# Performance work log

Measured on AMD Instinct MI355X. Metric: run time of the kernel, lower is better.

Reference implementation:

```python
import jax, jax.numpy as jnp
import numpy as np

N = 320      # points per coordinate axis
RANK = 64    # CP rank = features[-1]
H = 128      # hidden width
DIMS = 3     # input_dim


def setup_inputs() -> dict:
    key = jax.random.key(0)
    ks = jax.random.split(key, 6)
    s0 = (6.0 / (1 + H)) ** 0.5   # xavier-uniform-ish scale for 1->H
    s1 = (6.0 / (H + H)) ** 0.5
    s2 = (6.0 / (H + RANK)) ** 0.5
    return {
        "xs": jax.random.normal(ks[0], (DIMS, N, 1), dtype=jnp.float32),
        "W0": jax.random.uniform(ks[1], (DIMS, 1, H), jnp.float32, -s0, s0),
        "b0": jnp.zeros((DIMS, H), jnp.float32),
        "W1": jax.random.uniform(ks[2], (DIMS, H, H), jnp.float32, -s1, s1),
        "b1": jnp.zeros((DIMS, H), jnp.float32),
        "W2": jax.random.uniform(ks[3], (DIMS, H, H), jnp.float32, -s1, s1),
        "b2": jnp.zeros((DIMS, H), jnp.float32),
        "W3": jax.random.uniform(ks[4], (DIMS, H, RANK), jnp.float32, -s2, s2),
        "b3": jnp.zeros((DIMS, RANK), jnp.float32),
    }


def reference(xs, W0, b0, W1, b1, W2, b2, W3, b3):
    # Per-coordinate MLP (identical to independent Dense stacks in the flax loop),
    # vmapped over the DIMS leading axis of stacked params.
    def mlp(x, w0, bb0, w1, bb1, w2, bb2, w3, bb3):
        h = jnp.tanh(x @ w0 + bb0)          # (N, H)
        h = jnp.tanh(h @ w1 + bb1)          # (N, H)
        h = jnp.tanh(h @ w2 + bb2)          # (N, H)
        return h @ w3 + bb3                 # (N, R)

    outs = jax.vmap(mlp)(xs, W0, b0, W1, b1, W2, b2, W3, b3)  # (DIMS, N, R)
    f = jnp.transpose(outs, (0, 2, 1))                         # (DIMS, R, N)
    # CP reconstruction: 'ra,rb,rc->abc' over shared rank r
    return jnp.einsum('ra,rb,rc->abc', f[0], f[1], f[2])
```

## Files before the change

### kernel.cpp

```cpp
#include <hip/hip_runtime.h>
#include <math.h>

#define DIMS 3
#define NPTS 320
#define HID  128
#define RANK 64
#define CH   160
#define LROW 256

typedef __attribute__((ext_vector_type(8)))  short bf16x8;
typedef __attribute__((ext_vector_type(16))) float f32x16;

static __device__ __forceinline__ unsigned short f2bf_rn(float x) {
    union { float f; unsigned int u; } v; v.f = x;
    unsigned int r = v.u + 0x7fffu + ((v.u >> 16) & 1u);
    return (unsigned short)(r >> 16);
}
static __device__ __forceinline__ float bf2f(unsigned short h) {
    union { unsigned int u; float f; } v; v.u = ((unsigned int)h) << 16;
    return v.f;
}

__global__ __launch_bounds__(HID)
void mlp_kernel(const float* __restrict__ xs,
                const float* __restrict__ W0, const float* __restrict__ b0,
                const float* __restrict__ W1, const float* __restrict__ b1,
                const float* __restrict__ W2, const float* __restrict__ b2,
                const float* __restrict__ W3, const float* __restrict__ b3,
                float* __restrict__ f01t,
                unsigned short* __restrict__ f2hi,
                unsigned short* __restrict__ f2lo) {
    int blk = blockIdx.x;
    int d = blk / NPTS, n = blk % NPTS;
    int j = threadIdx.x;

    __shared__ float ha[HID];
    __shared__ float hb[HID];

    float x = xs[d * NPTS + n];

    ha[j] = tanhf(fmaf(x, W0[d * HID + j], b0[d * HID + j]));
    __syncthreads();

    {
        float acc = b1[d * HID + j];
        const float* w = W1 + d * HID * HID + j;
        #pragma unroll 16
        for (int k = 0; k < HID; ++k) acc = fmaf(ha[k], w[k * HID], acc);
        hb[j] = tanhf(acc);
    }
    __syncthreads();

    {
        float acc = b2[d * HID + j];
        const float* w = W2 + d * HID * HID + j;
        #pragma unroll 16
        for (int k = 0; k < HID; ++k) acc = fmaf(hb[k], w[k * HID], acc);
        ha[j] = tanhf(acc);
    }
    __syncthreads();

    if (j < RANK) {
        float acc = b3[d * RANK + j];
        const float* w = W3 + d * HID * RANK + j;
        #pragma unroll 16
        for (int k = 0; k < HID; ++k) acc = fmaf(ha[k], w[k * RANK], acc);

        if (d == 0) {
            f01t[n * RANK + j] = acc;
        } else if (d == 1) {
            f01t[(NPTS + n) * RANK + j] = acc;
        } else {
            unsigned short hi = f2bf_rn(acc);
            f2hi[n * RANK + j] = hi;
            f2lo[n * RANK + j] = f2bf_rn(acc - bf2f(hi));
        }
    }
}

__global__ __launch_bounds__(128, 2)
void cp_mfma_kernel(const float* __restrict__ f01t,
                    const unsigned short* __restrict__ f2hi,
                    const unsigned short* __restrict__ f2lo,
                    float* __restrict__ out) {
    const int tx = threadIdx.x;
    const int w  = tx >> 6;
    const int l  = tx & 63;
    const int lc = l & 31;
    const int hw = l >> 5;

    const int chalf = blockIdx.x & 1;
    const int c0 = chalf * CH;

    __shared__ char sB[CH * LROW];

    #pragma unroll
    for (int i = 0; i < 10; ++i) {
        int idx = tx + i * 128;
        int row = idx >> 3;
        int g   = (idx & 7) << 4;
        int sw  = (row & 15) << 4;
        *(float4*)(&sB[row * LROW + (g ^ sw)]) =
            ((const float4*)f2hi)[c0 * 8 + idx];
        *(float4*)(&sB[row * LROW + ((128 + g) ^ sw)]) =
            ((const float4*)f2lo)[c0 * 8 + idx];
    }
    __syncthreads();

    for (int t = blockIdx.x >> 1; t < NPTS * 5; t += 512) {
        const int a    = t / 5;
        const int b0w  = (t - a * 5) * 64 + w * 32;
        const float* f0p = f01t + (size_t)a * RANK + hw * 8;
        const float* f1p = f01t + (size_t)(NPTS + b0w + lc) * RANK + hw * 8;

        bf16x8 ahi[4], alo[4];
        #pragma unroll
        for (int ks = 0; ks < 4; ++ks) {
            const int k0 = ks * 16;
            float4 f0a = *(const float4*)(f0p + k0);
            float4 f0b = *(const float4*)(f0p + k0 + 4);
            float4 f1a = *(const float4*)(f1p + k0);
            float4 f1b = *(const float4*)(f1p + k0 + 4);

            float g[8];
            g[0] = f1a.x * f0a.x; g[1] = f1a.y * f0a.y;
            g[2] = f1a.z * f0a.z; g[3] = f1a.w * f0a.w;
            g[4] = f1b.x * f0b.x; g[5] = f1b.y * f0b.y;
            g[6] = f1b.z * f0b.z; g[7] = f1b.w * f0b.w;

            #pragma unroll
            for (int j = 0; j < 8; ++j) {
                unsigned short hi = f2bf_rn(g[j]);
                ahi[ks][j] = (short)hi;
                alo[ks][j] = (short)f2bf_rn(g[j] - bf2f(hi));
            }
        }

        #pragma unroll
        for (int ct = 0; ct < 5; ++ct) {
            const int lr = ct * 32 + lc;
            const int sw = (lr & 15) << 4;
            const char* rowp = &sB[lr * LROW];

            f32x16 acc;
            #pragma unroll
            for (int j = 0; j < 16; ++j) acc[j] = 0.0f;

            #pragma unroll
            for (int ks = 0; ks < 4; ++ks) {
                const int base = ks * 32 + (hw << 4);
                bf16x8 b_hi = *(const bf16x8*)(rowp + (base ^ sw));
                bf16x8 b_lo = *(const bf16x8*)(rowp + ((128 + base) ^ sw));
                acc = __builtin_amdgcn_mfma_f32_32x32x16_bf16(ahi[ks], b_hi, acc, 0, 0, 0);
                acc = __builtin_amdgcn_mfma_f32_32x32x16_bf16(ahi[ks], b_lo, acc, 0, 0, 0);
                acc = __builtin_amdgcn_mfma_f32_32x32x16_bf16(alo[ks], b_hi, acc, 0, 0, 0);
            }

            float* obase = out + ((size_t)a * NPTS + b0w) * NPTS + c0 + ct * 32 + lc;
            #pragma unroll
            for (int q = 0; q < 16; ++q) {
                int row = (q & 3) + 8 * (q >> 2) + 4 * hw;
                obase[(size_t)row * NPTS] = acc[q];
            }
        }
    }
}

extern "C" void kernel_launch(void* const* d_in, const int* in_sizes, int n_in,
                              void* d_out, int out_size, void* d_ws, size_t ws_size,
                              hipStream_t stream) {
    const float* xs = (const float*)d_in[0];
    const float* W0 = (const float*)d_in[1];
    const float* b0 = (const float*)d_in[2];
    const float* W1 = (const float*)d_in[3];
    const float* b1 = (const float*)d_in[4];
    const float* W2 = (const float*)d_in[5];
    const float* b2 = (const float*)d_in[6];
    const float* W3 = (const float*)d_in[7];
    const float* b3 = (const float*)d_in[8];

    float* f01t = (float*)d_ws;
    unsigned short* f2hi = (unsigned short*)((char*)d_ws + 2 * NPTS * RANK * 4);
    unsigned short* f2lo = f2hi + NPTS * RANK;
    float* out = (float*)d_out;

    mlp_kernel<<<dim3(DIMS * NPTS), dim3(HID), 0, stream>>>(
        xs, W0, b0, W1, b1, W2, b2, W3, b3, f01t, f2hi, f2lo);

    cp_mfma_kernel<<<dim3(1024), dim3(128), 0, stream>>>(f01t, f2hi, f2lo, out);
}
```

Measured before the change: 40.63 us.

## Widen CP blocks to four waves and split tiles contiguously per block

The CP reconstruction kernel now runs 256 threads per block. Each pair of waves covers two adjacent 'a' rows over a 64-wide b tile, so every shared-memory load of the f2 slice serves twice as much work. Blocks take contiguous ranges of tiles instead of a strided loop, which evens the per-block load and keeps output writes local. Two accumulators alternate across the column tiles so one tile's MFMAs can overlap the previous tile's stores, at the cost of more registers per thread.

```diff
diff --git a/kernel.cpp b/kernel.cpp
--- a/kernel.cpp
+++ b/kernel.cpp
@@ -78,25 +78,26 @@
     }
 }
 
-__global__ __launch_bounds__(128, 2)
+__global__ __launch_bounds__(256)
 void cp_mfma_kernel(const float* __restrict__ f01t,
                     const unsigned short* __restrict__ f2hi,
                     const unsigned short* __restrict__ f2lo,
                     float* __restrict__ out) {
     const int tx = threadIdx.x;
     const int w  = tx >> 6;
+    const int aw = w >> 1;
+    const int bw = (w & 1) * 32;
     const int l  = tx & 63;
     const int lc = l & 31;
     const int hw = l >> 5;
 
-    const int chalf = blockIdx.x & 1;
-    const int c0 = chalf * CH;
+    const int c0 = (blockIdx.x & 1) * CH;
 
     __shared__ char sB[CH * LROW];
 
     #pragma unroll
-    for (int i = 0; i < 10; ++i) {
-        int idx = tx + i * 128;
+    for (int i = 0; i < 5; ++i) {
+        int idx = tx + i * 256;
         int row = idx >> 3;
         int g   = (idx & 7) << 4;
         int sw  = (row & 15) << 4;
@@ -107,11 +108,18 @@
     }
     __syncthreads();
 
-    for (int t = blockIdx.x >> 1; t < NPTS * 5; t += 512) {
-        const int a    = t / 5;
-        const int b0w  = (t - a * 5) * 64 + w * 32;
+    const int slot   = blockIdx.x >> 1;
+    const int tstart = (slot * 25) >> 4;
+    const int tend   = ((slot + 1) * 25) >> 4;
+
+    for (int t = tstart; t < tend; ++t) {
+        const int apair = t / 5;
+        const int btile = t - apair * 5;
+        const int a  = apair * 2 + aw;
+        const int bb = btile * 64 + bw;
+
         const float* f0p = f01t + (size_t)a * RANK + hw * 8;
-        const float* f1p = f01t + (size_t)(NPTS + b0w + lc) * RANK + hw * 8;
+        const float* f1p = f01t + (size_t)(NPTS + bb + lc) * RANK + hw * 8;
 
         bf16x8 ahi[4], alo[4];
         #pragma unroll
@@ -136,33 +144,38 @@
             }
         }
 
-        #pragma unroll
-        for (int ct = 0; ct < 5; ++ct) {
-            const int lr = ct * 32 + lc;
-            const int sw = (lr & 15) << 4;
-            const char* rowp = &sB[lr * LROW];
-
-            f32x16 acc;
-            #pragma unroll
-            for (int j = 0; j < 16; ++j) acc[j] = 0.0f;
-
-            #pragma unroll
-            for (int ks = 0; ks < 4; ++ks) {
-                const int base = ks * 32 + (hw << 4);
-                bf16x8 b_hi = *(const bf16x8*)(rowp + (base ^ sw));
-                bf16x8 b_lo = *(const bf16x8*)(rowp + ((128 + base) ^ sw));
-                acc = __builtin_amdgcn_mfma_f32_32x32x16_bf16(ahi[ks], b_hi, acc, 0, 0, 0);
-                acc = __builtin_amdgcn_mfma_f32_32x32x16_bf16(ahi[ks], b_lo, acc, 0, 0, 0);
-                acc = __builtin_amdgcn_mfma_f32_32x32x16_bf16(alo[ks], b_hi, acc, 0, 0, 0);
-            }
-
-            float* obase = out + ((size_t)a * NPTS + b0w) * NPTS + c0 + ct * 32 + lc;
-            #pragma unroll
-            for (int q = 0; q < 16; ++q) {
-                int row = (q & 3) + 8 * (q >> 2) + 4 * hw;
-                obase[(size_t)row * NPTS] = acc[q];
-            }
+        float* obase = out + ((size_t)a * NPTS + bb) * NPTS + c0 + lc;
+
+#define CP_STEP(CT, ACC)                                                       \
+        {                                                                      \
+            const int lr = (CT) * 32 + lc;                                     \
+            const int sw2 = (lr & 15) << 4;                                    \
+            const char* rowp = &sB[lr * LROW];                                 \
+            _Pragma("unroll")                                                  \
+            for (int j = 0; j < 16; ++j) ACC[j] = 0.0f;                        \
+            _Pragma("unroll")                                                  \
+            for (int ks = 0; ks < 4; ++ks) {                                   \
+                const int base = ks * 32 + (hw << 4);                          \
+                bf16x8 b_hi = *(const bf16x8*)(rowp + (base ^ sw2));           \
+                bf16x8 b_lo = *(const bf16x8*)(rowp + ((128 + base) ^ sw2));   \
+                ACC = __builtin_amdgcn_mfma_f32_32x32x16_bf16(ahi[ks], b_hi, ACC, 0, 0, 0); \
+                ACC = __builtin_amdgcn_mfma_f32_32x32x16_bf16(ahi[ks], b_lo, ACC, 0, 0, 0); \
+                ACC = __builtin_amdgcn_mfma_f32_32x32x16_bf16(alo[ks], b_hi, ACC, 0, 0, 0); \
+            }                                                                  \
+            _Pragma("unroll")                                                  \
+            for (int q = 0; q < 16; ++q) {                                     \
+                int row = (q & 3) + 8 * (q >> 2) + 4 * hw;                     \
+                obase[(size_t)row * NPTS + (CT) * 32] = ACC[q];                \
+            }                                                                  \
         }
+
+        f32x16 accA, accB;
+        CP_STEP(0, accA)
+        CP_STEP(1, accB)
+        CP_STEP(2, accA)
+        CP_STEP(3, accB)
+        CP_STEP(4, accA)
+#undef CP_STEP
     }
 }
 
@@ -187,5 +200,5 @@
     mlp_kernel<<<dim3(DIMS * NPTS), dim3(HID), 0, stream>>>(
         xs, W0, b0, W1, b1, W2, b2, W3, b3, f01t, f2hi, f2lo);
 
-    cp_mfma_kernel<<<dim3(1024), dim3(128), 0, stream>>>(f01t, f2hi, f2lo, out);
-}
+    cp_mfma_kernel<<<dim3(1024), dim3(256), 0, stream>>>(f01t, f2hi, f2lo, out);
+}
```

Result: slower. 43.81 us (+7.8%).

## Batch MLP points per block and merge CP column halves into one block

Applied to the files above, without the earlier changes.

The MLP kernel now processes four points per block, so each weight load is reused across four accumulators and the block count drops by a factor of four. The CP kernel now uses 256-thread blocks that stage the full factor-2 matrix (80KB LDS) and split the column halves across warps. It also keeps five accumulators live so that all tile stores are issued together after the MFMAs. The costs are higher register pressure, large LDS use that limits occupancy, and fewer MLP blocks for the GPU to spread across its units.

```diff
diff --git a/kernel.cpp b/kernel.cpp
--- a/kernel.cpp
+++ b/kernel.cpp
@@ -5,8 +5,8 @@
 #define NPTS 320
 #define HID  128
 #define RANK 64
-#define CH   160
 #define LROW 256
+#define PB   4
 
 typedef __attribute__((ext_vector_type(8)))  short bf16x8;
 typedef __attribute__((ext_vector_type(16))) float f32x16;
@@ -30,88 +30,117 @@
                 float* __restrict__ f01t,
                 unsigned short* __restrict__ f2hi,
                 unsigned short* __restrict__ f2lo) {
-    int blk = blockIdx.x;
-    int d = blk / NPTS, n = blk % NPTS;
-    int j = threadIdx.x;
-
-    __shared__ float ha[HID];
-    __shared__ float hb[HID];
-
-    float x = xs[d * NPTS + n];
-
-    ha[j] = tanhf(fmaf(x, W0[d * HID + j], b0[d * HID + j]));
-    __syncthreads();
+    const int blk = blockIdx.x;
+    const int d  = blk / (NPTS / PB);
+    const int n0 = (blk - d * (NPTS / PB)) * PB;
+    const int j  = threadIdx.x;
+
+    __shared__ float ha[PB][HID];
+    __shared__ float hb[PB][HID];
+
+    float x[PB];
+    #pragma unroll
+    for (int p = 0; p < PB; ++p) x[p] = xs[d * NPTS + n0 + p];
 
     {
-        float acc = b1[d * HID + j];
+        float w = W0[d * HID + j], bb = b0[d * HID + j];
+        #pragma unroll
+        for (int p = 0; p < PB; ++p) ha[p][j] = tanhf(fmaf(x[p], w, bb));
+    }
+    __syncthreads();
+
+    {
+        float acc[PB];
+        #pragma unroll
+        for (int p = 0; p < PB; ++p) acc[p] = b1[d * HID + j];
         const float* w = W1 + d * HID * HID + j;
-        #pragma unroll 16
-        for (int k = 0; k < HID; ++k) acc = fmaf(ha[k], w[k * HID], acc);
-        hb[j] = tanhf(acc);
+        #pragma unroll 8
+        for (int k = 0; k < HID; ++k) {
+            float wv = w[k * HID];
+            #pragma unroll
+            for (int p = 0; p < PB; ++p) acc[p] = fmaf(ha[p][k], wv, acc[p]);
+        }
+        #pragma unroll
+        for (int p = 0; p < PB; ++p) hb[p][j] = tanhf(acc[p]);
     }
     __syncthreads();
 
     {
-        float acc = b2[d * HID + j];
+        float acc[PB];
+        #pragma unroll
+        for (int p = 0; p < PB; ++p) acc[p] = b2[d * HID + j];
         const float* w = W2 + d * HID * HID + j;
-        #pragma unroll 16
-        for (int k = 0; k < HID; ++k) acc = fmaf(hb[k], w[k * HID], acc);
-        ha[j] = tanhf(acc);
+        #pragma unroll 8
+        for (int k = 0; k < HID; ++k) {
+            float wv = w[k * HID];
+            #pragma unroll
+            for (int p = 0; p < PB; ++p) acc[p] = fmaf(hb[p][k], wv, acc[p]);
+        }
+        __syncthreads();
+        #pragma unroll
+        for (int p = 0; p < PB; ++p) ha[p][j] = tanhf(acc[p]);
     }
     __syncthreads();
 
     if (j < RANK) {
-        float acc = b3[d * RANK + j];
+        float acc[PB];
+        #pragma unroll
+        for (int p = 0; p < PB; ++p) acc[p] = b3[d * RANK + j];
         const float* w = W3 + d * HID * RANK + j;
-        #pragma unroll 16
-        for (int k = 0; k < HID; ++k) acc = fmaf(ha[k], w[k * RANK], acc);
-
-        if (d == 0) {
-            f01t[n * RANK + j] = acc;
-        } else if (d == 1) {
-            f01t[(NPTS + n) * RANK + j] = acc;
-        } else {
-            unsigned short hi = f2bf_rn(acc);
-            f2hi[n * RANK + j] = hi;
-            f2lo[n * RANK + j] = f2bf_rn(acc - bf2f(hi));
-        }
-    }
-}
-
-__global__ __launch_bounds__(128, 2)
+        #pragma unroll 8
+        for (int k = 0; k < HID; ++k) {
+            float wv = w[k * RANK];
+            #pragma unroll
+            for (int p = 0; p < PB; ++p) acc[p] = fmaf(ha[p][k], wv, acc[p]);
+        }
+        #pragma unroll
+        for (int p = 0; p < PB; ++p) {
+            int n = n0 + p;
+            if (d == 0) {
+                f01t[n * RANK + j] = acc[p];
+            } else if (d == 1) {
+                f01t[(NPTS + n) * RANK + j] = acc[p];
+            } else {
+                unsigned short hi = f2bf_rn(acc[p]);
+                f2hi[n * RANK + j] = hi;
+                f2lo[n * RANK + j] = f2bf_rn(acc[p] - bf2f(hi));
+            }
+        }
+    }
+}
+
+__global__ __launch_bounds__(256, 2)
 void cp_mfma_kernel(const float* __restrict__ f01t,
                     const unsigned short* __restrict__ f2hi,
                     const unsigned short* __restrict__ f2lo,
                     float* __restrict__ out) {
     const int tx = threadIdx.x;
     const int w  = tx >> 6;
+    const int bsub  = (w & 1) * 32;
+    const int chalf = (w >> 1) * 160;
     const int l  = tx & 63;
     const int lc = l & 31;
     const int hw = l >> 5;
 
-    const int chalf = blockIdx.x & 1;
-    const int c0 = chalf * CH;
-
-    __shared__ char sB[CH * LROW];
+    __shared__ char sB[NPTS * LROW];
 
     #pragma unroll
     for (int i = 0; i < 10; ++i) {
-        int idx = tx + i * 128;
+        int idx = tx + i * 256;
         int row = idx >> 3;
         int g   = (idx & 7) << 4;
         int sw  = (row & 15) << 4;
-        *(float4*)(&sB[row * LROW + (g ^ sw)]) =
-            ((const float4*)f2hi)[c0 * 8 + idx];
-        *(float4*)(&sB[row * LROW + ((128 + g) ^ sw)]) =
-            ((const float4*)f2lo)[c0 * 8 + idx];
-    }
-    __syncthreads();
-
-    for (int t = blockIdx.x >> 1; t < NPTS * 5; t += 512) {
-        const int a    = t / 5;
-        const int b0w  = (t - a * 5) * 64 + w * 32;
+        *(float4*)(&sB[row * LROW + (g ^ sw)])         = ((const float4*)f2hi)[idx];
+        *(float4*)(&sB[row * LROW + ((128 + g) ^ sw)]) = ((const float4*)f2lo)[idx];
+    }
+    __syncthreads();
+
+    for (int t = blockIdx.x; t < NPTS * 5; t += 512) {
+        const int a  = t / 5;
+        const int bb = (t - a * 5) * 64 + bsub;
+
         const float* f0p = f01t + (size_t)a * RANK + hw * 8;
-        const float* f1p = f01t + (size_t)(NPTS + b0w + lc) * RANK + hw * 8;
+        const float* f1p = f01t + (size_t)(NPTS + bb + lc) * RANK + hw * 8;
 
         bf16x8 ahi[4], alo[4];
         #pragma unroll
@@ -136,31 +165,35 @@
             }
         }
 
+        f32x16 acc[5];
         #pragma unroll
         for (int ct = 0; ct < 5; ++ct) {
-            const int lr = ct * 32 + lc;
-            const int sw = (lr & 15) << 4;
+            const int lr = chalf + ct * 32 + lc;
+            const int sw2 = (lr & 15) << 4;
             const char* rowp = &sB[lr * LROW];
 
-            f32x16 acc;
-            #pragma unroll
-            for (int j = 0; j < 16; ++j) acc[j] = 0.0f;
+            #pragma unroll
+            for (int jj = 0; jj < 16; ++jj) acc[ct][jj] = 0.0f;
 
             #pragma unroll
             for (int ks = 0; ks < 4; ++ks) {
                 const int base = ks * 32 + (hw << 4);
-                bf16x8 b_hi = *(const bf16x8*)(rowp + (base ^ sw));
-                bf16x8 b_lo = *(const bf16x8*)(rowp + ((128 + base) ^ sw));
-                acc = __builtin_amdgcn_mfma_f32_32x32x16_bf16(ahi[ks], b_hi, acc, 0, 0, 0);
-                acc = __builtin_amdgcn_mfma_f32_32x32x16_bf16(ahi[ks], b_lo, acc, 0, 0, 0);
-                acc = __builtin_amdgcn_mfma_f32_32x32x16_bf16(alo[ks], b_hi, acc, 0, 0, 0);
-            }
-
-            float* obase = out + ((size_t)a * NPTS + b0w) * NPTS + c0 + ct * 32 + lc;
-            #pragma unroll
-            for (int q = 0; q < 16; ++q) {
-                int row = (q & 3) + 8 * (q >> 2) + 4 * hw;
-                obase[(size_t)row * NPTS] = acc[q];
+                bf16x8 b_hi = *(const bf16x8*)(rowp + (base ^ sw2));
+                bf16x8 b_lo = *(const bf16x8*)(rowp + ((128 + base) ^ sw2));
+                acc[ct] = __builtin_amdgcn_mfma_f32_32x32x16_bf16(ahi[ks], b_hi, acc[ct], 0, 0, 0);
+                acc[ct] = __builtin_amdgcn_mfma_f32_32x32x16_bf16(ahi[ks], b_lo, acc[ct], 0, 0, 0);
+                acc[ct] = __builtin_amdgcn_mfma_f32_32x32x16_bf16(alo[ks], b_hi, acc[ct], 0, 0, 0);
+            }
+        }
+
+        float* obase = out + ((size_t)a * NPTS + bb) * NPTS + chalf + lc;
+        #pragma unroll
+        for (int q = 0; q < 16; ++q) {
+            const int row = (q & 3) + 8 * (q >> 2) + 4 * hw;
+            float* orow = obase + (size_t)row * NPTS;
+            #pragma unroll
+            for (int ct = 0; ct < 5; ++ct) {
+                orow[ct * 32] = acc[ct][q];
             }
         }
     }
@@ -184,8 +217,8 @@
     unsigned short* f2lo = f2hi + NPTS * RANK;
     float* out = (float*)d_out;
 
-    mlp_kernel<<<dim3(DIMS * NPTS), dim3(HID), 0, stream>>>(
+    mlp_kernel<<<dim3(DIMS * NPTS / PB), dim3(HID), 0, stream>>>(
         xs, W0, b0, W1, b1, W2, b2, W3, b3, f01t, f2hi, f2lo);
 
-    cp_mfma_kernel<<<dim3(1024), dim3(128), 0, stream>>>(f01t, f2hi, f2lo, out);
-}
+    cp_mfma_kernel<<<dim3(512), dim3(256), 0, stream>>>(f01t, f2hi, f2lo, out);
+}
```

Result: slower. 57.63 us (+41.8%).
